# Optimization experiments

Measured on AMD Instinct MI355X. Metric: run time of the kernel, lower is better.

Reference implementation:

```python
import jax, jax.numpy as jnp
import numpy as np

N_NODES = 100000
N_EDGES = 640000
NUM_GRAPHS = 256
IN_DIM, HID_DIM, OUT_DIM = 128, 128, 64


def setup_inputs() -> dict:
    key = jax.random.key(0)
    ks = jax.random.split(key, 6)
    x = jax.random.normal(ks[0], (N_NODES, IN_DIM), dtype=jnp.float32)
    edge_index = jax.random.randint(ks[1], (2, N_EDGES), 0, N_NODES, dtype=jnp.int64)
    batch = jnp.sort(jax.random.randint(ks[2], (N_NODES,), 0, NUM_GRAPHS, dtype=jnp.int64))
    W1 = jax.random.normal(ks[3], (IN_DIM, HID_DIM), dtype=jnp.float32) * (1.0 / np.sqrt(IN_DIM))
    b1 = jnp.zeros((HID_DIM,), dtype=jnp.float32)
    W2 = jax.random.normal(ks[4], (HID_DIM, OUT_DIM), dtype=jnp.float32) * (1.0 / np.sqrt(HID_DIM))
    b2 = jnp.zeros((OUT_DIM,), dtype=jnp.float32)
    return {"x": x, "edge_index": edge_index, "batch": batch,
            "W1": W1, "b1": b1, "W2": W2, "b2": b2}


def gcn_conv(x, row, col, norm, W, b, n_nodes):
    # transform first (smaller of in/out handled by W), then gather-scale-scatter
    xw = x @ W                                   # [N, F_out]
    msgs = norm[:, None] * xw[row]               # [E+N, F_out]
    out = jax.ops.segment_sum(msgs, col, num_segments=n_nodes)
    return out + b


def reference(x, edge_index, batch, W1, b1, W2, b2):
    n = x.shape[0]
    # add self-loops (PyG GCNConv default)
    loops = jnp.arange(n, dtype=edge_index.dtype)
    row = jnp.concatenate([edge_index[0], loops])  # sources
    col = jnp.concatenate([edge_index[1], loops])  # targets
    # symmetric normalization D^-1/2 (A+I) D^-1/2
    deg = jax.ops.segment_sum(jnp.ones_like(col, dtype=x.dtype), col, num_segments=n)
    dinv = jnp.where(deg > 0, jax.lax.rsqrt(deg), 0.0)
    norm = dinv[row] * dinv[col]
    h = jax.nn.relu(gcn_conv(x, row, col, norm, W1, b1, n))
    h = gcn_conv(h, row, col, norm, W2, b2, n)
    # global mean pool over batch ids
    sums = jax.ops.segment_sum(h, batch, num_segments=NUM_GRAPHS)
    counts = jax.ops.segment_sum(jnp.ones((n,), dtype=h.dtype), batch, num_segments=NUM_GRAPHS)
    return sums / jnp.clip(counts, 1.0)[:, None]
```

## Files before the change

kernel.cpp:

```cpp
#include <hip/hip_runtime.h>
#include <hip/hip_bf16.h>


__device__ __forceinline__ void atomAddF(float* p, float v) {
  unsafeAtomicAdd(p, v);
}

__global__ __launch_bounds__(256) void k_count(const int* __restrict__ col,
                                               int* __restrict__ deg, int E) {
  int e = blockIdx.x * 256 + threadIdx.x;
  if (e < E) atomicAdd(&deg[col[e]], 1);
}

__global__ __launch_bounds__(256) void k_blocksum(const int* __restrict__ deg,
                                                  int* __restrict__ partial, int N) {
  __shared__ int sh[256];
  int t = threadIdx.x, i = blockIdx.x * 256 + t;
  sh[t] = (i < N) ? deg[i] : 0;
  __syncthreads();
  for (int o = 128; o > 0; o >>= 1) {
    if (t < o) sh[t] += sh[t + o];
    __syncthreads();
  }
  if (t == 0) partial[blockIdx.x] = sh[0];
}

__global__ __launch_bounds__(512) void k_scanpartial(int* __restrict__ partial, int nb) {
  __shared__ int sh[512];
  int t = threadIdx.x;
  int v = (t < nb) ? partial[t] : 0;
  sh[t] = v;
  __syncthreads();
  for (int o = 1; o < 512; o <<= 1) {
    int x = (t >= o) ? sh[t - o] : 0;
    __syncthreads();
    sh[t] += x;
    __syncthreads();
  }
  if (t < nb) partial[t] = sh[t] - v;
}

__global__ __launch_bounds__(256) void k_scanblock(int* __restrict__ deg,
    const int* __restrict__ partial, int* __restrict__ off,
    float* __restrict__ dinv, int N) {
  __shared__ int sh[256];
  int t = threadIdx.x, b = blockIdx.x, i = b * 256 + t;
  int v = (i < N) ? deg[i] : 0;
  sh[t] = v;
  __syncthreads();
  for (int o = 1; o < 256; o <<= 1) {
    int x = (t >= o) ? sh[t - o] : 0;
    __syncthreads();
    sh[t] += x;
    __syncthreads();
  }
  if (i < N) {
    int excl = partial[b] + sh[t] - v;
    off[i] = excl;
    deg[i] = excl;
    dinv[i] = rsqrtf((float)v + 1.0f);
    if (i == N - 1) off[N] = excl + v;
  }
}

__global__ __launch_bounds__(256) void k_fillcsr(const int* __restrict__ rows,
    const int* __restrict__ cols, int* __restrict__ cursor,
    int* __restrict__ csrsrc, int E) {
  int e = blockIdx.x * 256 + threadIdx.x;
  if (e < E) {
    int pos = atomicAdd(&cursor[cols[e]], 1);
    csrsrc[pos] = rows[e];
  }
}

__global__ __launch_bounds__(256) void k_goff(const int* __restrict__ batch,
                                              int* __restrict__ goff, int N, int G) {
  int g = blockIdx.x * 256 + threadIdx.x;
  if (g > G) return;
  int lo = 0, hi = N;
  while (lo < hi) {
    int m = (lo + hi) >> 1;
    if (batch[m] < g) lo = m + 1; else hi = m;
  }
  goff[g] = lo;
}

__global__ __launch_bounds__(256) void k_gemm1(
    const float* __restrict__ x, const float* __restrict__ W,
    const float* __restrict__ dinv, float* __restrict__ y, int N)
{
  __shared__ float Xt[128][36];
  __shared__ float Wl[128][64];
  const int tid = threadIdx.x;
  const int v0 = blockIdx.x * 32;

  {
    int vn = tid >> 3;
    int c0 = (tid & 7) << 4;
    int vv = v0 + vn; if (vv >= N) vv = N - 1;
    const float4* xr = (const float4*)(x + (size_t)vv * 128 + c0);
#pragma unroll
    for (int i = 0; i < 4; ++i) {
      float4 t = xr[i];
      int k = c0 + (i << 2);
      Xt[k + 0][vn] = t.x; Xt[k + 1][vn] = t.y; Xt[k + 2][vn] = t.z; Xt[k + 3][vn] = t.w;
    }
  }

  const int cg = tid & 15;
  const int ng = tid >> 4;
  const int va = v0 + 2 * ng, vb = va + 1;
  const float dva = dinv[va < N ? va : N - 1];
  const float dvb = dinv[vb < N ? vb : N - 1];

  for (int h = 0; h < 2; ++h) {
    __syncthreads();
    {
      const float4* Wg = (const float4*)W;
      for (int idx = tid; idx < 2048; idx += 256) {
        int r = idx >> 4, q = idx & 15;
        ((float4*)&Wl[r][0])[q] = Wg[r * 32 + (h << 4) + q];
      }
    }
    __syncthreads();
    float ca[4] = {0.f, 0.f, 0.f, 0.f}, cb[4] = {0.f, 0.f, 0.f, 0.f};
    for (int k = 0; k < 128; ++k) {
      float2 a = *(const float2*)&Xt[k][ng << 1];
      float4 w = *(const float4*)&Wl[k][cg << 2];
      ca[0] += a.x * w.x; ca[1] += a.x * w.y; ca[2] += a.x * w.z; ca[3] += a.x * w.w;
      cb[0] += a.y * w.x; cb[1] += a.y * w.y; cb[2] += a.y * w.z; cb[3] += a.y * w.w;
    }
    if (va < N) {
      size_t base = (size_t)va * 128 + (h << 6) + (cg << 2);
      *(float4*)(y + base) = make_float4(dva * ca[0], dva * ca[1], dva * ca[2], dva * ca[3]);
    }
    if (vb < N) {
      size_t base = (size_t)vb * 128 + (h << 6) + (cg << 2);
      *(float4*)(y + base) = make_float4(dvb * cb[0], dvb * cb[1], dvb * cb[2], dvb * cb[3]);
    }
  }
}

__global__ __launch_bounds__(256) void k_gemm2_fused(
    const float* __restrict__ y, const int* __restrict__ off, const int* __restrict__ src,
    const float* __restrict__ W, const float* __restrict__ dinv,
    const float* __restrict__ b1, float* __restrict__ z, int N)
{
  __shared__ float Xt[128][36];
  __shared__ float Wl[128][64];
  const int tid = threadIdx.x;
  const int v0 = blockIdx.x * 32;

  {
    const float4* Wg = (const float4*)W;
    for (int idx = tid; idx < 2048; idx += 256) {
      int r = idx >> 4, q = idx & 15;
      ((float4*)&Wl[r][0])[q] = Wg[r * 16 + q];
    }
  }
  {
    int vn = tid >> 3;
    int c0 = (tid & 7) << 4;
    int vv = v0 + vn;
    int vc = (vv < N) ? vv : N - 1;
    float acc[16];
    const float4* yr = (const float4*)(y + (size_t)vc * 128 + c0);
#pragma unroll
    for (int q = 0; q < 4; ++q) {
      float4 t = yr[q];
      acc[4*q+0] = t.x; acc[4*q+1] = t.y; acc[4*q+2] = t.z; acc[4*q+3] = t.w;
    }
    int e0 = off[vc], e1 = off[vc + 1];
    int last = e1 - 1;
    for (int i = e0; i < e1; i += 4) {
      int i1 = i + 1, i2 = i + 2, i3 = i + 3;
      int u0 = src[i];
      int u1 = src[i1 <= last ? i1 : last];
      int u2 = src[i2 <= last ? i2 : last];
      int u3 = src[i3 <= last ? i3 : last];
      float m1 = (i1 <= last) ? 1.f : 0.f;
      float m2 = (i2 <= last) ? 1.f : 0.f;
      float m3 = (i3 <= last) ? 1.f : 0.f;
      const float4* p0 = (const float4*)(y + (size_t)u0 * 128 + c0);
      const float4* p1 = (const float4*)(y + (size_t)u1 * 128 + c0);
      const float4* p2 = (const float4*)(y + (size_t)u2 * 128 + c0);
      const float4* p3 = (const float4*)(y + (size_t)u3 * 128 + c0);
#pragma unroll
      for (int q = 0; q < 4; ++q) {
        float4 t0 = p0[q], t1 = p1[q], t2 = p2[q], t3 = p3[q];
        acc[4*q+0] += t0.x + m1 * t1.x + m2 * t2.x + m3 * t3.x;
        acc[4*q+1] += t0.y + m1 * t1.y + m2 * t2.y + m3 * t3.y;
        acc[4*q+2] += t0.z + m1 * t1.z + m2 * t2.z + m3 * t3.z;
        acc[4*q+3] += t0.w + m1 * t1.w + m2 * t2.w + m3 * t3.w;
      }
    }
    float d = dinv[vc];
#pragma unroll
    for (int j = 0; j < 16; ++j)
      Xt[c0 + j][vn] = fmaxf(fmaf(d, acc[j], b1[c0 + j]), 0.f);
  }
  __syncthreads();

  const int cg = tid & 15;
  const int ng = tid >> 4;
  const int va = v0 + 2 * ng, vb = va + 1;
  const float dva = dinv[va < N ? va : N - 1];
  const float dvb = dinv[vb < N ? vb : N - 1];

  float ca[4] = {0.f, 0.f, 0.f, 0.f}, cb[4] = {0.f, 0.f, 0.f, 0.f};
  for (int k = 0; k < 128; ++k) {
    float2 a = *(const float2*)&Xt[k][ng << 1];
    float4 w = *(const float4*)&Wl[k][cg << 2];
    ca[0] += a.x * w.x; ca[1] += a.x * w.y; ca[2] += a.x * w.z; ca[3] += a.x * w.w;
    cb[0] += a.y * w.x; cb[1] += a.y * w.y; cb[2] += a.y * w.z; cb[3] += a.y * w.w;
  }
  if (va < N) {
    size_t base = (size_t)va * 64 + (cg << 2);
    *(float4*)(z + base) = make_float4(dva * ca[0], dva * ca[1], dva * ca[2], dva * ca[3]);
  }
  if (vb < N) {
    size_t base = (size_t)vb * 64 + (cg << 2);
    *(float4*)(z + base) = make_float4(dvb * cb[0], dvb * cb[1], dvb * cb[2], dvb * cb[3]);
  }
}

__global__ __launch_bounds__(256) void k_aggpool(
    const float* __restrict__ z, const int* __restrict__ off, const int* __restrict__ src,
    const float* __restrict__ dinv, const int* __restrict__ goff,
    float* __restrict__ out, int N)
{
  int g = blockIdx.x >> 3, seg = blockIdx.x & 7;
  int w = threadIdx.x >> 6, lane = threadIdx.x & 63;
  int lo = goff[g], hi = goff[g + 1];
  float acc = 0.f;
  for (int v = lo + seg * 4 + w; v < hi; v += 32) {
    float sv = z[(size_t)v * 64 + lane];
    int e0 = off[v], e1 = off[v + 1];
    int last = e1 - 1;
    for (int i = e0; i < e1; i += 4) {
      int i1 = i + 1, i2 = i + 2, i3 = i + 3;
      int u0 = src[i];
      int u1 = src[i1 <= last ? i1 : last];
      int u2 = src[i2 <= last ? i2 : last];
      int u3 = src[i3 <= last ? i3 : last];
      float a0 = z[(size_t)u0 * 64 + lane];
      float a1 = z[(size_t)u1 * 64 + lane];
      float a2 = z[(size_t)u2 * 64 + lane];
      float a3 = z[(size_t)u3 * 64 + lane];
      sv += a0;
      sv += (i1 <= last) ? a1 : 0.f;
      sv += (i2 <= last) ? a2 : 0.f;
      sv += (i3 <= last) ? a3 : 0.f;
    }
    acc = fmaf(dinv[v], sv, acc);
  }
  atomAddF(out + (size_t)g * 64 + lane, acc);
}

__global__ __launch_bounds__(256) void k_final(float* __restrict__ out,
    const int* __restrict__ goff, const float* __restrict__ b2, int total) {
  int i = blockIdx.x * 256 + threadIdx.x;
  if (i >= total) return;
  int g = i >> 6, d = i & 63;
  int n = goff[g + 1] - goff[g];
  out[i] = (n > 0) ? out[i] / (float)n + b2[d] : 0.f;
}

extern "C" void kernel_launch(void* const* d_in, const int* in_sizes, int n_in,
                              void* d_out, int out_size, void* d_ws, size_t ws_size,
                              hipStream_t stream) {
  const float* x     = (const float*)d_in[0];
  const int*   eidx  = (const int*)d_in[1];
  const int*   batch = (const int*)d_in[2];
  const float* W1    = (const float*)d_in[3];
  const float* b1    = (const float*)d_in[4];
  const float* W2    = (const float*)d_in[5];
  const float* b2    = (const float*)d_in[6];
  float* out = (float*)d_out;

  const int N = in_sizes[2];
  const int E = in_sizes[1] / 2;
  const int G = out_size / 64;

  const int* rows = eidx;
  const int* cols = eidx + E;

  float* ybuf   = (float*)d_ws;
  float* zbuf   = ybuf + (size_t)N * 128;
  float* dinv   = zbuf + (size_t)N * 64;
  int*   deg    = (int*)(dinv + N);
  int*   off    = deg + N;
  int*   partial= off + N + 1;
  int*   goff   = partial + 512;
  int*   csrsrc = goff + G + 1;

  const int B = 256;
  const int nb = (N + B - 1) / B;

  hipMemsetAsync(deg, 0, (size_t)N * sizeof(int), stream);
  hipMemsetAsync(d_out, 0, (size_t)out_size * sizeof(float), stream);

  k_count<<<(E + B - 1) / B, B, 0, stream>>>(cols, deg, E);
  k_blocksum<<<nb, B, 0, stream>>>(deg, partial, N);
  k_scanpartial<<<1, 512, 0, stream>>>(partial, nb);
  k_scanblock<<<nb, B, 0, stream>>>(deg, partial, off, dinv, N);
  k_fillcsr<<<(E + B - 1) / B, B, 0, stream>>>(rows, cols, deg, csrsrc, E);
  k_goff<<<(G + 1 + B - 1) / B, B, 0, stream>>>(batch, goff, N, G);

  k_gemm1<<<(N + 31) / 32, B, 0, stream>>>(x, W1, dinv, ybuf, N);
  k_gemm2_fused<<<(N + 31) / 32, B, 0, stream>>>(ybuf, off, csrsrc, W2, dinv, b1, zbuf, N);
  k_aggpool<<<G * 8, B, 0, stream>>>(zbuf, off, csrsrc, dinv, goff, out, N);
  k_final<<<(out_size + B - 1) / B, B, 0, stream>>>(out, goff, b2, out_size);
}
```

Baseline: 338.5 us.

## Use split-bf16 MFMA matrix cores for both GCN feature transforms

Replaces the scalar FP32 shared-memory GEMMs with MFMA 16x16x32 bf16 instructions. A three-term hi/lo bf16 split keeps accuracy close to FP32. Weights are pre-split and transposed by a new prep kernel. The second GEMM now stages the aggregated hidden features as swizzled bf16 hi/lo tiles in LDS, and its gather loop is reshaped to 4 threads per node with 2-edge unrolling. The change adds conversion work and tripled MFMA count, and may reduce memory-level parallelism in the gather.

```diff
diff --git a/kernel.cpp b/kernel.cpp
--- a/kernel.cpp
+++ b/kernel.cpp
@@ -2,8 +2,38 @@
 #include <hip/hip_bf16.h>
 
 
-__device__ __forceinline__ void atomAddF(float* p, float v) {
-  unsafeAtomicAdd(p, v);
+typedef __attribute__((ext_vector_type(8))) short short8;
+typedef __attribute__((ext_vector_type(4))) float f32x4;
+
+__device__ __forceinline__ void atomAddF(float* p, float v) { unsafeAtomicAdd(p, v); }
+
+__device__ __forceinline__ unsigned short bf_rne(float f) {
+  unsigned int u = __float_as_uint(f);
+  return (unsigned short)((u + 0x7fffu + ((u >> 16) & 1u)) >> 16);
+}
+__device__ __forceinline__ float bf2f(unsigned short h) {
+  return __uint_as_float(((unsigned int)h) << 16);
+}
+
+__global__ __launch_bounds__(256) void k_prepw(const float* __restrict__ W1,
+    const float* __restrict__ W2,
+    unsigned short* __restrict__ W1th, unsigned short* __restrict__ W1tl,
+    unsigned short* __restrict__ W2th, unsigned short* __restrict__ W2tl) {
+  int i = blockIdx.x * 256 + threadIdx.x;
+  if (i < 16384) {
+    int c = i >> 7, k = i & 127;
+    float f = W1[k * 128 + c];
+    unsigned short hi = bf_rne(f);
+    W1th[i] = hi;
+    W1tl[i] = bf_rne(f - bf2f(hi));
+  } else if (i < 16384 + 8192) {
+    int j = i - 16384;
+    int c = j >> 7, k = j & 127;
+    float f = W2[k * 64 + c];
+    unsigned short hi = bf_rne(f);
+    W2th[j] = hi;
+    W2tl[j] = bf_rne(f - bf2f(hi));
+  }
 }
 
 __global__ __launch_bounds__(256) void k_count(const int* __restrict__ col,
@@ -85,149 +115,178 @@
   goff[g] = lo;
 }
 
-__global__ __launch_bounds__(256) void k_gemm1(
-    const float* __restrict__ x, const float* __restrict__ W,
+__global__ __launch_bounds__(256) void k_gemm1_mfma(
+    const float* __restrict__ x,
+    const unsigned short* __restrict__ W1th, const unsigned short* __restrict__ W1tl,
     const float* __restrict__ dinv, float* __restrict__ y, int N)
 {
-  __shared__ float Xt[128][36];
-  __shared__ float Wl[128][64];
   const int tid = threadIdx.x;
-  const int v0 = blockIdx.x * 32;
-
+  const int w = tid >> 6, l = tid & 63;
+  const int v0 = blockIdx.x * 64;
+  const int l15 = l & 15, lh = l >> 4;
+
+  short8 bh[2][4], bl[2][4];
+#pragma unroll
+  for (int ct = 0; ct < 2; ++ct) {
+    int colr = 32 * w + 16 * ct + l15;
+#pragma unroll
+    for (int ks = 0; ks < 4; ++ks) {
+      bh[ct][ks] = *(const short8*)(W1th + colr * 128 + ks * 32 + 8 * lh);
+      bl[ct][ks] = *(const short8*)(W1tl + colr * 128 + ks * 32 + 8 * lh);
+    }
+  }
+
+#pragma unroll
+  for (int rt = 0; rt < 4; ++rt) {
+    int arow = v0 + rt * 16 + l15; if (arow >= N) arow = N - 1;
+    const float* ar = x + (size_t)arow * 128 + 8 * lh;
+    f32x4 acc0 = {0.f, 0.f, 0.f, 0.f}, acc1 = {0.f, 0.f, 0.f, 0.f};
+#pragma unroll
+    for (int ks = 0; ks < 4; ++ks) {
+      float4 fa = *(const float4*)(ar + ks * 32);
+      float4 fb = *(const float4*)(ar + ks * 32 + 4);
+      short8 ah, al;
+      float v0f;
+      v0f = fa.x; ah[0] = (short)bf_rne(v0f); al[0] = (short)bf_rne(v0f - bf2f((unsigned short)ah[0]));
+      v0f = fa.y; ah[1] = (short)bf_rne(v0f); al[1] = (short)bf_rne(v0f - bf2f((unsigned short)ah[1]));
+      v0f = fa.z; ah[2] = (short)bf_rne(v0f); al[2] = (short)bf_rne(v0f - bf2f((unsigned short)ah[2]));
+      v0f = fa.w; ah[3] = (short)bf_rne(v0f); al[3] = (short)bf_rne(v0f - bf2f((unsigned short)ah[3]));
+      v0f = fb.x; ah[4] = (short)bf_rne(v0f); al[4] = (short)bf_rne(v0f - bf2f((unsigned short)ah[4]));
+      v0f = fb.y; ah[5] = (short)bf_rne(v0f); al[5] = (short)bf_rne(v0f - bf2f((unsigned short)ah[5]));
+      v0f = fb.z; ah[6] = (short)bf_rne(v0f); al[6] = (short)bf_rne(v0f - bf2f((unsigned short)ah[6]));
+      v0f = fb.w; ah[7] = (short)bf_rne(v0f); al[7] = (short)bf_rne(v0f - bf2f((unsigned short)ah[7]));
+      acc0 = __builtin_amdgcn_mfma_f32_16x16x32_bf16(ah, bh[0][ks], acc0, 0, 0, 0);
+      acc0 = __builtin_amdgcn_mfma_f32_16x16x32_bf16(al, bh[0][ks], acc0, 0, 0, 0);
+      acc0 = __builtin_amdgcn_mfma_f32_16x16x32_bf16(ah, bl[0][ks], acc0, 0, 0, 0);
+      acc1 = __builtin_amdgcn_mfma_f32_16x16x32_bf16(ah, bh[1][ks], acc1, 0, 0, 0);
+      acc1 = __builtin_amdgcn_mfma_f32_16x16x32_bf16(al, bh[1][ks], acc1, 0, 0, 0);
+      acc1 = __builtin_amdgcn_mfma_f32_16x16x32_bf16(ah, bl[1][ks], acc1, 0, 0, 0);
+    }
+
+    int r4 = v0 + rt * 16 + lh * 4;
+    float4 d4 = *(const float4*)(dinv + r4);
+    int col0 = 32 * w + l15;
+#pragma unroll
+    for (int reg = 0; reg < 4; ++reg) {
+      int row = r4 + reg;
+      if (row < N) {
+        float dd = (reg == 0) ? d4.x : (reg == 1) ? d4.y : (reg == 2) ? d4.z : d4.w;
+        y[(size_t)row * 128 + col0]      = acc0[reg] * dd;
+        y[(size_t)row * 128 + col0 + 16] = acc1[reg] * dd;
+      }
+    }
+  }
+}
+
+__global__ __launch_bounds__(256) void k_gemm2_fused_mfma(
+    const float* __restrict__ y, const int* __restrict__ off,
+    const int* __restrict__ src,
+    const unsigned short* __restrict__ W2th, const unsigned short* __restrict__ W2tl,
+    const float* __restrict__ dinv, const float* __restrict__ b1,
+    float* __restrict__ z, int N)
+{
+  __shared__ unsigned short hh[64 * 128];
+  __shared__ unsigned short hl[64 * 128];
+  const int tid = threadIdx.x;
+  const int w = tid >> 6, l = tid & 63;
+  const int v0 = blockIdx.x * 64;
+  const int l15 = l & 15, lh = l >> 4;
+
+  short8 bh[4], bl[4];
   {
-    int vn = tid >> 3;
-    int c0 = (tid & 7) << 4;
-    int vv = v0 + vn; if (vv >= N) vv = N - 1;
-    const float4* xr = (const float4*)(x + (size_t)vv * 128 + c0);
-#pragma unroll
-    for (int i = 0; i < 4; ++i) {
-      float4 t = xr[i];
-      int k = c0 + (i << 2);
-      Xt[k + 0][vn] = t.x; Xt[k + 1][vn] = t.y; Xt[k + 2][vn] = t.z; Xt[k + 3][vn] = t.w;
-    }
-  }
-
-  const int cg = tid & 15;
-  const int ng = tid >> 4;
-  const int va = v0 + 2 * ng, vb = va + 1;
-  const float dva = dinv[va < N ? va : N - 1];
-  const float dvb = dinv[vb < N ? vb : N - 1];
-
-  for (int h = 0; h < 2; ++h) {
-    __syncthreads();
-    {
-      const float4* Wg = (const float4*)W;
-      for (int idx = tid; idx < 2048; idx += 256) {
-        int r = idx >> 4, q = idx & 15;
-        ((float4*)&Wl[r][0])[q] = Wg[r * 32 + (h << 4) + q];
-      }
-    }
-    __syncthreads();
-    float ca[4] = {0.f, 0.f, 0.f, 0.f}, cb[4] = {0.f, 0.f, 0.f, 0.f};
-    for (int k = 0; k < 128; ++k) {
-      float2 a = *(const float2*)&Xt[k][ng << 1];
-      float4 w = *(const float4*)&Wl[k][cg << 2];
-      ca[0] += a.x * w.x; ca[1] += a.x * w.y; ca[2] += a.x * w.z; ca[3] += a.x * w.w;
-      cb[0] += a.y * w.x; cb[1] += a.y * w.y; cb[2] += a.y * w.z; cb[3] += a.y * w.w;
-    }
-    if (va < N) {
-      size_t base = (size_t)va * 128 + (h << 6) + (cg << 2);
-      *(float4*)(y + base) = make_float4(dva * ca[0], dva * ca[1], dva * ca[2], dva * ca[3]);
-    }
-    if (vb < N) {
-      size_t base = (size_t)vb * 128 + (h << 6) + (cg << 2);
-      *(float4*)(y + base) = make_float4(dvb * cb[0], dvb * cb[1], dvb * cb[2], dvb * cb[3]);
-    }
-  }
-}
-
-__global__ __launch_bounds__(256) void k_gemm2_fused(
-    const float* __restrict__ y, const int* __restrict__ off, const int* __restrict__ src,
-    const float* __restrict__ W, const float* __restrict__ dinv,
-    const float* __restrict__ b1, float* __restrict__ z, int N)
-{
-  __shared__ float Xt[128][36];
-  __shared__ float Wl[128][64];
-  const int tid = threadIdx.x;
-  const int v0 = blockIdx.x * 32;
+    int colr = 16 * w + l15;
+#pragma unroll
+    for (int ks = 0; ks < 4; ++ks) {
+      bh[ks] = *(const short8*)(W2th + colr * 128 + ks * 32 + 8 * lh);
+      bl[ks] = *(const short8*)(W2tl + colr * 128 + ks * 32 + 8 * lh);
+    }
+  }
 
   {
-    const float4* Wg = (const float4*)W;
-    for (int idx = tid; idx < 2048; idx += 256) {
-      int r = idx >> 4, q = idx & 15;
-      ((float4*)&Wl[r][0])[q] = Wg[r * 16 + q];
-    }
-  }
-  {
-    int vn = tid >> 3;
-    int c0 = (tid & 7) << 4;
+    int vn = tid >> 2;
+    int c0 = (tid & 3) * 32;
     int vv = v0 + vn;
     int vc = (vv < N) ? vv : N - 1;
-    float acc[16];
-    const float4* yr = (const float4*)(y + (size_t)vc * 128 + c0);
-#pragma unroll
-    for (int q = 0; q < 4; ++q) {
-      float4 t = yr[q];
-      acc[4*q+0] = t.x; acc[4*q+1] = t.y; acc[4*q+2] = t.z; acc[4*q+3] = t.w;
+    float acc[32];
+    {
+      const float4* yr = (const float4*)(y + (size_t)vc * 128 + c0);
+#pragma unroll
+      for (int q = 0; q < 8; ++q) {
+        float4 t = yr[q];
+        acc[4*q+0] = t.x; acc[4*q+1] = t.y; acc[4*q+2] = t.z; acc[4*q+3] = t.w;
+      }
     }
     int e0 = off[vc], e1 = off[vc + 1];
     int last = e1 - 1;
-    for (int i = e0; i < e1; i += 4) {
-      int i1 = i + 1, i2 = i + 2, i3 = i + 3;
+    for (int i = e0; i < e1; i += 2) {
+      int i1 = i + 1;
       int u0 = src[i];
       int u1 = src[i1 <= last ? i1 : last];
-      int u2 = src[i2 <= last ? i2 : last];
-      int u3 = src[i3 <= last ? i3 : last];
       float m1 = (i1 <= last) ? 1.f : 0.f;
-      float m2 = (i2 <= last) ? 1.f : 0.f;
-      float m3 = (i3 <= last) ? 1.f : 0.f;
       const float4* p0 = (const float4*)(y + (size_t)u0 * 128 + c0);
       const float4* p1 = (const float4*)(y + (size_t)u1 * 128 + c0);
-      const float4* p2 = (const float4*)(y + (size_t)u2 * 128 + c0);
-      const float4* p3 = (const float4*)(y + (size_t)u3 * 128 + c0);
-#pragma unroll
-      for (int q = 0; q < 4; ++q) {
-        float4 t0 = p0[q], t1 = p1[q], t2 = p2[q], t3 = p3[q];
-        acc[4*q+0] += t0.x + m1 * t1.x + m2 * t2.x + m3 * t3.x;
-        acc[4*q+1] += t0.y + m1 * t1.y + m2 * t2.y + m3 * t3.y;
-        acc[4*q+2] += t0.z + m1 * t1.z + m2 * t2.z + m3 * t3.z;
-        acc[4*q+3] += t0.w + m1 * t1.w + m2 * t2.w + m3 * t3.w;
+#pragma unroll
+      for (int q = 0; q < 8; ++q) {
+        float4 t0 = p0[q], t1 = p1[q];
+        acc[4*q+0] += t0.x + m1 * t1.x;
+        acc[4*q+1] += t0.y + m1 * t1.y;
+        acc[4*q+2] += t0.z + m1 * t1.z;
+        acc[4*q+3] += t0.w + m1 * t1.w;
       }
     }
     float d = dinv[vc];
 #pragma unroll
-    for (int j = 0; j < 16; ++j)
-      Xt[c0 + j][vn] = fmaxf(fmaf(d, acc[j], b1[c0 + j]), 0.f);
+    for (int s = 0; s < 4; ++s) {
+      short8 oh, ol;
+#pragma unroll
+      for (int j = 0; j < 8; ++j) {
+        int dim = c0 + s * 8 + j;
+        float hv = fmaxf(fmaf(d, acc[s*8+j], b1[dim]), 0.f);
+        unsigned short hb = bf_rne(hv);
+        oh[j] = (short)hb;
+        ol[j] = (short)bf_rne(hv - bf2f(hb));
+      }
+      int byte = (vn * 256 + (c0 + s * 8) * 2) ^ ((vn & 7) << 4);
+      *(short8*)((char*)hh + byte) = oh;
+      *(short8*)((char*)hl + byte) = ol;
+    }
   }
   __syncthreads();
 
-  const int cg = tid & 15;
-  const int ng = tid >> 4;
-  const int va = v0 + 2 * ng, vb = va + 1;
-  const float dva = dinv[va < N ? va : N - 1];
-  const float dvb = dinv[vb < N ? vb : N - 1];
-
-  float ca[4] = {0.f, 0.f, 0.f, 0.f}, cb[4] = {0.f, 0.f, 0.f, 0.f};
-  for (int k = 0; k < 128; ++k) {
-    float2 a = *(const float2*)&Xt[k][ng << 1];
-    float4 w = *(const float4*)&Wl[k][cg << 2];
-    ca[0] += a.x * w.x; ca[1] += a.x * w.y; ca[2] += a.x * w.z; ca[3] += a.x * w.w;
-    cb[0] += a.y * w.x; cb[1] += a.y * w.y; cb[2] += a.y * w.z; cb[3] += a.y * w.w;
-  }
-  if (va < N) {
-    size_t base = (size_t)va * 64 + (cg << 2);
-    *(float4*)(z + base) = make_float4(dva * ca[0], dva * ca[1], dva * ca[2], dva * ca[3]);
-  }
-  if (vb < N) {
-    size_t base = (size_t)vb * 64 + (cg << 2);
-    *(float4*)(z + base) = make_float4(dvb * cb[0], dvb * cb[1], dvb * cb[2], dvb * cb[3]);
+#pragma unroll
+  for (int rt = 0; rt < 4; ++rt) {
+    int row = rt * 16 + l15;
+    const int swz = (row & 7) << 4;
+    const int base = row * 256 + lh * 16;
+    f32x4 acc = {0.f, 0.f, 0.f, 0.f};
+#pragma unroll
+    for (int ks = 0; ks < 4; ++ks) {
+      int byte = (base + ks * 64) ^ swz;
+      short8 ah = *(const short8*)((char*)hh + byte);
+      short8 al = *(const short8*)((char*)hl + byte);
+      acc = __builtin_amdgcn_mfma_f32_16x16x32_bf16(ah, bh[ks], acc, 0, 0, 0);
+      acc = __builtin_amdgcn_mfma_f32_16x16x32_bf16(al, bh[ks], acc, 0, 0, 0);
+      acc = __builtin_amdgcn_mfma_f32_16x16x32_bf16(ah, bl[ks], acc, 0, 0, 0);
+    }
+
+    int r4 = v0 + rt * 16 + lh * 4;
+    float4 d4 = *(const float4*)(dinv + r4);
+    int col = 16 * w + l15;
+#pragma unroll
+    for (int reg = 0; reg < 4; ++reg) {
+      int rr = r4 + reg;
+      if (rr < N) {
+        float dd = (reg == 0) ? d4.x : (reg == 1) ? d4.y : (reg == 2) ? d4.z : d4.w;
+        z[(size_t)rr * 64 + col] = acc[reg] * dd;
+      }
+    }
   }
 }
 
 __global__ __launch_bounds__(256) void k_aggpool(
-    const float* __restrict__ z, const int* __restrict__ off, const int* __restrict__ src,
-    const float* __restrict__ dinv, const int* __restrict__ goff,
-    float* __restrict__ out, int N)
+    const float* __restrict__ z, const int* __restrict__ off,
+    const int* __restrict__ src, const float* __restrict__ dinv,
+    const int* __restrict__ goff, float* __restrict__ out, int N)
 {
   int g = blockIdx.x >> 3, seg = blockIdx.x & 7;
   int w = threadIdx.x >> 6, lane = threadIdx.x & 63;
@@ -285,20 +344,26 @@
   const int* rows = eidx;
   const int* cols = eidx + E;
 
-  float* ybuf   = (float*)d_ws;
-  float* zbuf   = ybuf + (size_t)N * 128;
-  float* dinv   = zbuf + (size_t)N * 64;
-  int*   deg    = (int*)(dinv + N);
-  int*   off    = deg + N;
-  int*   partial= off + N + 1;
-  int*   goff   = partial + 512;
-  int*   csrsrc = goff + G + 1;
+  float* y   = (float*)d_ws;
+  float* z   = y + (size_t)N * 128;
+  unsigned short* W1th = (unsigned short*)(z + (size_t)N * 64);
+  unsigned short* W1tl = W1th + 16384;
+  unsigned short* W2th = W1tl + 16384;
+  unsigned short* W2tl = W2th + 8192;
+  float* dinv    = (float*)(W2tl + 8192);
+  int*   deg     = (int*)(dinv + N);
+  int*   off     = deg + N;
+  int*   partial = off + N + 1;
+  int*   goff    = partial + 512;
+  int*   csrsrc  = goff + G + 1;
 
   const int B = 256;
   const int nb = (N + B - 1) / B;
 
   hipMemsetAsync(deg, 0, (size_t)N * sizeof(int), stream);
   hipMemsetAsync(d_out, 0, (size_t)out_size * sizeof(float), stream);
+
+  k_prepw<<<(16384 + 8192 + B - 1) / B, B, 0, stream>>>(W1, W2, W1th, W1tl, W2th, W2tl);
 
   k_count<<<(E + B - 1) / B, B, 0, stream>>>(cols, deg, E);
   k_blocksum<<<nb, B, 0, stream>>>(deg, partial, N);
@@ -307,8 +372,8 @@
   k_fillcsr<<<(E + B - 1) / B, B, 0, stream>>>(rows, cols, deg, csrsrc, E);
   k_goff<<<(G + 1 + B - 1) / B, B, 0, stream>>>(batch, goff, N, G);
 
-  k_gemm1<<<(N + 31) / 32, B, 0, stream>>>(x, W1, dinv, ybuf, N);
-  k_gemm2_fused<<<(N + 31) / 32, B, 0, stream>>>(ybuf, off, csrsrc, W2, dinv, b1, zbuf, N);
-  k_aggpool<<<G * 8, B, 0, stream>>>(zbuf, off, csrsrc, dinv, goff, out, N);
+  k_gemm1_mfma<<<(N + 63) / 64, B, 0, stream>>>(x, W1th, W1tl, dinv, y, N);
+  k_gemm2_fused_mfma<<<(N + 63) / 64, B, 0, stream>>>(y, off, csrsrc, W2th, W2tl, dinv, b1, z, N);
+  k_aggpool<<<G * 8, B, 0, stream>>>(z, off, csrsrc, dinv, goff, out, N);
   k_final<<<(out_size + B - 1) / B, B, 0, stream>>>(out, goff, b2, out_size);
 }
```

Result: slower. 355.3 us (+5.0%).
